# Optimization experiments

Measured on AMD Instinct MI355X. Metric: run time of the kernel, lower is better.

## Reference

```python
import jax, jax.numpy as jnp
import numpy as np

D_MODEL = 1024
D_K = 1024
B = 4
T = 2048

def setup_inputs() -> dict:
    key = jax.random.key(0)
    k_x, k_q, k_k, k_v = jax.random.split(key, 4)
    s = 1.0 / np.sqrt(D_MODEL)
    return {
        "x": jax.random.normal(k_x, (B, T, D_MODEL), dtype=jnp.float32),
        "Wq": jax.random.normal(k_q, (D_MODEL, D_K), dtype=jnp.float32) * s,
        "Wk": jax.random.normal(k_k, (D_MODEL, D_K), dtype=jnp.float32) * s,
        "Wv": jax.random.normal(k_v, (D_MODEL, D_K), dtype=jnp.float32) * s,
    }

def reference(x, Wq, Wk, Wv):
    # x: (B, T, d_model); Wq/Wk/Wv: (d_model, d_k)
    Q = jnp.einsum('btd,dk->btk', x, Wq)
    K = jnp.einsum('btd,dk->btk', x, Wk)
    V = jnp.einsum('btd,dk->btk', x, Wv)
    scale = 1.0 / jnp.sqrt(jnp.asarray(D_K, dtype=x.dtype))
    scores = jnp.einsum('bqk,bsk->bqs', Q, K) * scale  # (B, T, T)
    t = scores.shape[1]
    causal = jnp.triu(jnp.ones((t, t), dtype=bool), k=1)  # True above diagonal
    scores = jnp.where(causal[None, :, :], jnp.asarray(-jnp.inf, dtype=scores.dtype), scores)
    weights = jax.nn.softmax(scores, axis=-1)
    # dropout p=0.0 -> identity
    return jnp.einsum('bqs,bsk->bqk', weights, V)
```

## Files before the change

kernel.cpp:

```cpp
#include <hip/hip_runtime.h>
#include <cstdint>

typedef __attribute__((ext_vector_type(4))) float f32x4;
typedef __attribute__((ext_vector_type(8))) __bf16 bf16x8;
typedef __attribute__((ext_vector_type(8))) unsigned short u16x8;

__device__ __forceinline__ unsigned short f2bf(float f) {
    union { float f; unsigned u; } v; v.f = f;
    unsigned u = v.u + 0x7FFFu + ((v.u >> 16) & 1u);
    return (unsigned short)(u >> 16);
}
__device__ __forceinline__ float bf2f(unsigned short h) {
    union { unsigned u; float f; } v; v.u = ((unsigned)h) << 16;
    return v.f;
}

__device__ __forceinline__ void gld_lds16(const void* g, void* l) {
    auto gp = reinterpret_cast<const __attribute__((address_space(1))) unsigned int*>(
        reinterpret_cast<uintptr_t>(g));
    auto lp = reinterpret_cast<__attribute__((address_space(3))) unsigned int*>(
        reinterpret_cast<uintptr_t>(l));
    __builtin_amdgcn_global_load_lds(gp, lp, 16, 0, 0);
}

template<int BF16OUT>
__device__ __forceinline__ void gemm_core(
    const unsigned short* A, int lda,
    const unsigned short* B, int ldb,
    void* C, int ldc,
    int ktiles, float scale,
    unsigned short* lA, unsigned short* lB)
{
    const int t = threadIdx.x;
    const int l = t & 63;
    const int w = t >> 6;
    const int wr = w >> 1, wc = w & 1;

    f32x4 acc[4][4];
#pragma unroll
    for (int i = 0; i < 4; ++i)
#pragma unroll
        for (int j = 0; j < 4; ++j)
#pragma unroll
            for (int e = 0; e < 4; ++e) acc[i][j][e] = 0.f;

    const int srow = t >> 3;
    const int schunk = t & 7;

    for (int kt = 0; kt < ktiles; ++kt) {
        const int k0 = kt << 6;
#pragma unroll
        for (int p = 0; p < 4; ++p) {
            const int row = (p << 5) + srow;
            const int sc = schunk ^ (row & 7);
            gld_lds16(A + (size_t)row * lda + k0 + (sc << 3), lA + (p << 11) + (t << 3));
            gld_lds16(B + (size_t)row * ldb + k0 + (sc << 3), lB + (p << 11) + (t << 3));
        }
        __syncthreads();
#pragma unroll
        for (int kk = 0; kk < 2; ++kk) {
            bf16x8 af[4], bfr[4];
            const int c = (kk << 5) + ((l >> 4) << 3);
#pragma unroll
            for (int mf = 0; mf < 4; ++mf) {
                const int r = (wr << 6) + (mf << 4) + (l & 15);
                const int ad = ((r << 6) + c) ^ ((r & 7) << 3);
                af[mf] = *(const bf16x8*)(lA + ad);
            }
#pragma unroll
            for (int nf = 0; nf < 4; ++nf) {
                const int r = (wc << 6) + (nf << 4) + (l & 15);
                const int ad = ((r << 6) + c) ^ ((r & 7) << 3);
                bfr[nf] = *(const bf16x8*)(lB + ad);
            }
#pragma unroll
            for (int mf = 0; mf < 4; ++mf)
#pragma unroll
                for (int nf = 0; nf < 4; ++nf)
                    acc[mf][nf] = __builtin_amdgcn_mfma_f32_16x16x32_bf16(
                        af[mf], bfr[nf], acc[mf][nf], 0, 0, 0);
        }
        __syncthreads();
    }

#pragma unroll
    for (int mf = 0; mf < 4; ++mf)
#pragma unroll
        for (int nf = 0; nf < 4; ++nf)
#pragma unroll
            for (int j = 0; j < 4; ++j) {
                const int row = (wr << 6) + (mf << 4) + ((l >> 4) << 2) + j;
                const int col = (wc << 6) + (nf << 4) + (l & 15);
                const float v = acc[mf][nf][j] * scale;
                if (BF16OUT)
                    ((unsigned short*)C)[(size_t)row * ldc + col] = f2bf(v);
                else
                    ((float*)C)[(size_t)row * ldc + col] = v;
            }
}

__global__ __launch_bounds__(256) void k_gemm_proj(
    const unsigned short* __restrict__ xb, const unsigned short* __restrict__ wt,
    unsigned short* __restrict__ out, float scale)
{
    __shared__ unsigned short lA[8192], lB[8192];
    gemm_core<1>(xb + (size_t)blockIdx.y * 128 * 1024, 1024,
                 wt + (size_t)blockIdx.x * 128 * 1024, 1024,
                 out + (size_t)blockIdx.y * 128 * 1024 + blockIdx.x * 128, 1024,
                 16, scale, lA, lB);
}

__global__ __launch_bounds__(256) void k_gemm_vt(
    const unsigned short* __restrict__ wtv, const unsigned short* __restrict__ xb,
    unsigned short* __restrict__ vt)
{
    __shared__ unsigned short lA[8192], lB[8192];
    gemm_core<1>(wtv + (size_t)blockIdx.y * 128 * 1024, 1024,
                 xb + (size_t)blockIdx.x * 128 * 1024, 1024,
                 vt + (size_t)blockIdx.y * 128 * 8192 + blockIdx.x * 128, 8192,
                 16, 1.0f, lA, lB);
}

__global__ __launch_bounds__(256) void k_scores(
    const unsigned short* __restrict__ Qb, const unsigned short* __restrict__ Kb,
    unsigned short* __restrict__ S)
{
    const int kt = blockIdx.x, qt = blockIdx.y, b = blockIdx.z;
    if (kt > qt) return;
    __shared__ unsigned short lA[8192], lB[8192];
    gemm_core<1>(Qb + ((size_t)b * 2048 + qt * 128) * 1024, 1024,
                 Kb + ((size_t)b * 2048 + kt * 128) * 1024, 1024,
                 S + (size_t)b * 4194304 + (size_t)qt * 128 * 2048 + kt * 128, 2048,
                 16, 1.0f, lA, lB);
}

__global__ __launch_bounds__(256) void k_pv(
    const unsigned short* __restrict__ P, const unsigned short* __restrict__ Vt,
    float* __restrict__ out)
{
    const int dn = blockIdx.x, qt = blockIdx.y, b = blockIdx.z;
    __shared__ unsigned short lA[8192], lB[8192];
    gemm_core<0>(P + (size_t)b * 4194304 + (size_t)qt * 128 * 2048, 2048,
                 Vt + (size_t)dn * 128 * 8192 + b * 2048, 8192,
                 out + ((size_t)b * 2048 + qt * 128) * 1024 + dn * 128, 1024,
                 (qt + 1) * 2, 1.0f, lA, lB);
}

__global__ __launch_bounds__(256) void k_cast_bf16(
    const float* __restrict__ in, unsigned short* __restrict__ out, int n8)
{
    const int i = blockIdx.x * 256 + threadIdx.x;
    if (i >= n8) return;
    const float4* p = (const float4*)in + (size_t)i * 2;
    const float4 a = p[0], b = p[1];
    u16x8 r;
    r[0] = f2bf(a.x); r[1] = f2bf(a.y); r[2] = f2bf(a.z); r[3] = f2bf(a.w);
    r[4] = f2bf(b.x); r[5] = f2bf(b.y); r[6] = f2bf(b.z); r[7] = f2bf(b.w);
    *(u16x8*)(out + (size_t)i * 8) = r;
}

__global__ __launch_bounds__(256) void k_transpose_cast(
    const float* __restrict__ in, unsigned short* __restrict__ out)
{
    __shared__ float tile[32][33];
    const int bx = blockIdx.x * 32, by = blockIdx.y * 32;
    const int tx = threadIdx.x, ty = threadIdx.y;
    for (int r = ty; r < 32; r += 8)
        tile[r][tx] = in[(size_t)(by + r) * 1024 + bx + tx];
    __syncthreads();
    for (int r = ty; r < 32; r += 8)
        out[(size_t)(bx + r) * 1024 + by + tx] = f2bf(tile[tx][r]);
}

__global__ __launch_bounds__(256) void k_softmax(unsigned short* __restrict__ S)
{
    const int w = threadIdx.x >> 6, l = threadIdx.x & 63;
    const int r = blockIdx.x * 4 + w;
    const int b = r >> 11, lr = r & 2047;
    unsigned short* row = S + ((size_t)b << 22) + ((size_t)lr << 11);
    const int edge = ((lr >> 7) + 1) << 7;

    float v[32];
#pragma unroll
    for (int i = 0; i < 4; ++i) {
        const int c0 = (l << 3) + (i << 9);
        if (c0 < edge) {
            const u16x8 u = *(const u16x8*)(row + c0);
#pragma unroll
            for (int j = 0; j < 8; ++j)
                v[(i << 3) + j] = (c0 + j <= lr) ? bf2f(u[j]) : -3.0e38f;
        } else {
#pragma unroll
            for (int j = 0; j < 8; ++j) v[(i << 3) + j] = -3.0e38f;
        }
    }
    float m = v[0];
#pragma unroll
    for (int k = 1; k < 32; ++k) m = fmaxf(m, v[k]);
#pragma unroll
    for (int s = 32; s; s >>= 1) m = fmaxf(m, __shfl_xor(m, s, 64));
    float sum = 0.f;
#pragma unroll
    for (int k = 0; k < 32; ++k) { const float e = __expf(v[k] - m); v[k] = e; sum += e; }
#pragma unroll
    for (int s = 32; s; s >>= 1) sum += __shfl_xor(sum, s, 64);
    const float inv = 1.f / sum;
#pragma unroll
    for (int i = 0; i < 4; ++i) {
        const int c0 = (l << 3) + (i << 9);
        if (c0 < edge) {
            u16x8 o;
#pragma unroll
            for (int j = 0; j < 8; ++j) o[j] = f2bf(v[(i << 3) + j] * inv);
            *(u16x8*)(row + c0) = o;
        }
    }
}

extern "C" void kernel_launch(void* const* d_in, const int* in_sizes, int n_in,
                              void* d_out, int out_size, void* d_ws, size_t ws_size,
                              hipStream_t stream)
{
    (void)in_sizes; (void)n_in; (void)out_size; (void)ws_size;
    const float* x  = (const float*)d_in[0];
    const float* Wq = (const float*)d_in[1];
    const float* Wk = (const float*)d_in[2];
    const float* Wv = (const float*)d_in[3];
    float* out = (float*)d_out;

    char* w = (char*)d_ws;
    unsigned short* xb  = (unsigned short*)(w);
    unsigned short* wtq = (unsigned short*)(w + 16777216);
    unsigned short* wtk = (unsigned short*)(w + 18874368);
    unsigned short* wtv = (unsigned short*)(w + 20971520);
    unsigned short* Qb  = (unsigned short*)(w + 23068672);
    unsigned short* Kb  = (unsigned short*)(w + 39845888);
    unsigned short* Vt  = (unsigned short*)(w + 56623104);
    unsigned short* S   = (unsigned short*)(w + 73400320);

    k_cast_bf16<<<4096, 256, 0, stream>>>(x, xb, 1048576);
    const dim3 tb(32, 8);
    k_transpose_cast<<<dim3(32, 32), tb, 0, stream>>>(Wq, wtq);
    k_transpose_cast<<<dim3(32, 32), tb, 0, stream>>>(Wk, wtk);
    k_transpose_cast<<<dim3(32, 32), tb, 0, stream>>>(Wv, wtv);

    k_gemm_proj<<<dim3(8, 64), 256, 0, stream>>>(xb, wtq, Qb, 0.03125f);
    k_gemm_proj<<<dim3(8, 64), 256, 0, stream>>>(xb, wtk, Kb, 1.0f);
    k_gemm_vt <<<dim3(64, 8), 256, 0, stream>>>(wtv, xb, Vt);

    k_scores  <<<dim3(16, 16, 4), 256, 0, stream>>>(Qb, Kb, S);
    k_softmax <<<2048, 256, 0, stream>>>(S);
    k_pv      <<<dim3(8, 16, 4), 256, 0, stream>>>(S, Vt, out);
}
```

Measured before the change: 267.9 us.

## Double-buffer GEMM core with 512 threads, fuse QK projection, balance PV tiles

```diff
diff --git a/kernel.cpp b/kernel.cpp
--- a/kernel.cpp
+++ b/kernel.cpp
@@ -24,11 +24,11 @@
 }
 
 template<int BF16OUT>
-__device__ __forceinline__ void gemm_core(
-    const unsigned short* A, int lda,
-    const unsigned short* B, int ldb,
-    void* C, int ldc,
-    int ktiles, float scale,
+__device__ __forceinline__ void gemm8(
+    const unsigned short* __restrict__ A, int lda,
+    const unsigned short* __restrict__ B, int ldb,
+    void* __restrict__ C, int ldc,
+    int ktiles,
     unsigned short* lA, unsigned short* lB)
 {
     const int t = threadIdx.x;
@@ -36,62 +36,74 @@
     const int w = t >> 6;
     const int wr = w >> 1, wc = w & 1;
 
-    f32x4 acc[4][4];
-#pragma unroll
-    for (int i = 0; i < 4; ++i)
+    f32x4 acc[2][4];
+#pragma unroll
+    for (int i = 0; i < 2; ++i)
 #pragma unroll
         for (int j = 0; j < 4; ++j)
 #pragma unroll
             for (int e = 0; e < 4; ++e) acc[i][j][e] = 0.f;
 
-    const int srow = t >> 3;
-    const int schunk = t & 7;
-
-    for (int kt = 0; kt < ktiles; ++kt) {
+    auto stage = [&](int p, int kt) {
         const int k0 = kt << 6;
 #pragma unroll
-        for (int p = 0; p < 4; ++p) {
-            const int row = (p << 5) + srow;
-            const int sc = schunk ^ (row & 7);
-            gld_lds16(A + (size_t)row * lda + k0 + (sc << 3), lA + (p << 11) + (t << 3));
-            gld_lds16(B + (size_t)row * ldb + k0 + (sc << 3), lB + (p << 11) + (t << 3));
-        }
-        __syncthreads();
+        for (int i = 0; i < 2; ++i) {
+            const int flat = t + (i << 9);
+            const int row = flat >> 3;
+            const int sc = (flat & 7) ^ (row & 7);
+            gld_lds16(A + (size_t)row * lda + k0 + (sc << 3), lA + (p << 13) + (flat << 3));
+            gld_lds16(B + (size_t)row * ldb + k0 + (sc << 3), lB + (p << 13) + (flat << 3));
+        }
+    };
+
+    auto compute = [&](int p) {
 #pragma unroll
         for (int kk = 0; kk < 2; ++kk) {
-            bf16x8 af[4], bfr[4];
+            bf16x8 af[2], bfr[4];
             const int c = (kk << 5) + ((l >> 4) << 3);
 #pragma unroll
-            for (int mf = 0; mf < 4; ++mf) {
-                const int r = (wr << 6) + (mf << 4) + (l & 15);
-                const int ad = ((r << 6) + c) ^ ((r & 7) << 3);
+            for (int mf = 0; mf < 2; ++mf) {
+                const int r = (wr << 5) + (mf << 4) + (l & 15);
+                const int ad = (((r << 6) + c) ^ ((r & 7) << 3)) + (p << 13);
                 af[mf] = *(const bf16x8*)(lA + ad);
             }
 #pragma unroll
             for (int nf = 0; nf < 4; ++nf) {
                 const int r = (wc << 6) + (nf << 4) + (l & 15);
-                const int ad = ((r << 6) + c) ^ ((r & 7) << 3);
+                const int ad = (((r << 6) + c) ^ ((r & 7) << 3)) + (p << 13);
                 bfr[nf] = *(const bf16x8*)(lB + ad);
             }
-#pragma unroll
-            for (int mf = 0; mf < 4; ++mf)
+            __builtin_amdgcn_s_setprio(1);
+#pragma unroll
+            for (int mf = 0; mf < 2; ++mf)
 #pragma unroll
                 for (int nf = 0; nf < 4; ++nf)
                     acc[mf][nf] = __builtin_amdgcn_mfma_f32_16x16x32_bf16(
                         af[mf], bfr[nf], acc[mf][nf], 0, 0, 0);
-        }
+            __builtin_amdgcn_s_setprio(0);
+        }
+    };
+
+    stage(0, 0);
+    __syncthreads();
+    int p = 0;
+    for (int kt = 0; kt < ktiles - 1; ++kt) {
+        stage(p ^ 1, kt + 1);
+        compute(p);
         __syncthreads();
+        p ^= 1;
     }
-
-#pragma unroll
-    for (int mf = 0; mf < 4; ++mf)
+    compute(p);
+
+#pragma unroll
+    for (int mf = 0; mf < 2; ++mf)
 #pragma unroll
         for (int nf = 0; nf < 4; ++nf)
 #pragma unroll
             for (int j = 0; j < 4; ++j) {
-                const int row = (wr << 6) + (mf << 4) + ((l >> 4) << 2) + j;
+                const int row = (wr << 5) + (mf << 4) + ((l >> 4) << 2) + j;
                 const int col = (wc << 6) + (nf << 4) + (l & 15);
-                const float v = acc[mf][nf][j] * scale;
+                const float v = acc[mf][nf][j];
                 if (BF16OUT)
                     ((unsigned short*)C)[(size_t)row * ldc + col] = f2bf(v);
                 else
@@ -99,51 +111,56 @@
             }
 }
 
-__global__ __launch_bounds__(256) void k_gemm_proj(
-    const unsigned short* __restrict__ xb, const unsigned short* __restrict__ wt,
-    unsigned short* __restrict__ out, float scale)
-{
-    __shared__ unsigned short lA[8192], lB[8192];
-    gemm_core<1>(xb + (size_t)blockIdx.y * 128 * 1024, 1024,
-                 wt + (size_t)blockIdx.x * 128 * 1024, 1024,
-                 out + (size_t)blockIdx.y * 128 * 1024 + blockIdx.x * 128, 1024,
-                 16, scale, lA, lB);
-}
-
-__global__ __launch_bounds__(256) void k_gemm_vt(
+__global__ __launch_bounds__(512, 4) void k_gemm_qk(
+    const unsigned short* __restrict__ xb, const unsigned short* __restrict__ wtqk,
+    unsigned short* __restrict__ qk)
+{
+    __shared__ unsigned short lA[16384], lB[16384];
+    gemm8<1>(xb + (size_t)blockIdx.y * 128 * 1024, 1024,
+             wtqk + (size_t)blockIdx.x * 128 * 1024, 1024,
+             qk + (size_t)blockIdx.y * 128 * 2048 + blockIdx.x * 128, 2048,
+             16, lA, lB);
+}
+
+__global__ __launch_bounds__(512, 4) void k_gemm_vt(
     const unsigned short* __restrict__ wtv, const unsigned short* __restrict__ xb,
     unsigned short* __restrict__ vt)
 {
-    __shared__ unsigned short lA[8192], lB[8192];
-    gemm_core<1>(wtv + (size_t)blockIdx.y * 128 * 1024, 1024,
-                 xb + (size_t)blockIdx.x * 128 * 1024, 1024,
-                 vt + (size_t)blockIdx.y * 128 * 8192 + blockIdx.x * 128, 8192,
-                 16, 1.0f, lA, lB);
-}
-
-__global__ __launch_bounds__(256) void k_scores(
-    const unsigned short* __restrict__ Qb, const unsigned short* __restrict__ Kb,
-    unsigned short* __restrict__ S)
+    __shared__ unsigned short lA[16384], lB[16384];
+    gemm8<1>(wtv + (size_t)blockIdx.y * 128 * 1024, 1024,
+             xb + (size_t)blockIdx.x * 128 * 1024, 1024,
+             vt + (size_t)blockIdx.y * 128 * 8192 + blockIdx.x * 128, 8192,
+             16, lA, lB);
+}
+
+__global__ __launch_bounds__(512, 4) void k_scores(
+    const unsigned short* __restrict__ qk, unsigned short* __restrict__ S)
 {
     const int kt = blockIdx.x, qt = blockIdx.y, b = blockIdx.z;
     if (kt > qt) return;
-    __shared__ unsigned short lA[8192], lB[8192];
-    gemm_core<1>(Qb + ((size_t)b * 2048 + qt * 128) * 1024, 1024,
-                 Kb + ((size_t)b * 2048 + kt * 128) * 1024, 1024,
-                 S + (size_t)b * 4194304 + (size_t)qt * 128 * 2048 + kt * 128, 2048,
-                 16, 1.0f, lA, lB);
-}
-
-__global__ __launch_bounds__(256) void k_pv(
+    __shared__ unsigned short lA[16384], lB[16384];
+    gemm8<1>(qk + ((size_t)b * 2048 + qt * 128) * 2048, 2048,
+             qk + ((size_t)b * 2048 + kt * 128) * 2048 + 1024, 2048,
+             S + (size_t)b * 4194304 + (size_t)qt * 128 * 2048 + kt * 128, 2048,
+             16, lA, lB);
+}
+
+__global__ __launch_bounds__(512, 4) void k_pv(
     const unsigned short* __restrict__ P, const unsigned short* __restrict__ Vt,
     float* __restrict__ out)
 {
-    const int dn = blockIdx.x, qt = blockIdx.y, b = blockIdx.z;
-    __shared__ unsigned short lA[8192], lB[8192];
-    gemm_core<0>(P + (size_t)b * 4194304 + (size_t)qt * 128 * 2048, 2048,
-                 Vt + (size_t)dn * 128 * 8192 + b * 2048, 8192,
-                 out + ((size_t)b * 2048 + qt * 128) * 1024 + dn * 128, 1024,
-                 (qt + 1) * 2, 1.0f, lA, lB);
+    const int dn = blockIdx.x, pr = blockIdx.y, b = blockIdx.z;
+    __shared__ unsigned short lA[16384], lB[16384];
+    const int q1 = pr, q2 = 15 - pr;
+    gemm8<0>(P + (size_t)b * 4194304 + (size_t)q1 * 128 * 2048, 2048,
+             Vt + (size_t)dn * 128 * 8192 + b * 2048, 8192,
+             out + ((size_t)b * 2048 + q1 * 128) * 1024 + dn * 128, 1024,
+             (q1 + 1) * 2, lA, lB);
+    __syncthreads();
+    gemm8<0>(P + (size_t)b * 4194304 + (size_t)q2 * 128 * 2048, 2048,
+             Vt + (size_t)dn * 128 * 8192 + b * 2048, 8192,
+             out + ((size_t)b * 2048 + q2 * 128) * 1024 + dn * 128, 1024,
+             (q2 + 1) * 2, lA, lB);
 }
 
 __global__ __launch_bounds__(256) void k_cast_bf16(
@@ -159,17 +176,22 @@
     *(u16x8*)(out + (size_t)i * 8) = r;
 }
 
-__global__ __launch_bounds__(256) void k_transpose_cast(
-    const float* __restrict__ in, unsigned short* __restrict__ out)
+__global__ __launch_bounds__(256) void k_transpose3(
+    const float* __restrict__ Wq, const float* __restrict__ Wk, const float* __restrict__ Wv,
+    unsigned short* __restrict__ wtqk, unsigned short* __restrict__ wtv)
 {
     __shared__ float tile[32][33];
+    const int z = blockIdx.z;
+    const float* in = (z == 0) ? Wq : (z == 1) ? Wk : Wv;
+    unsigned short* out = (z < 2) ? (wtqk + (size_t)z * 1048576) : wtv;
+    const float s = (z == 0) ? 0.03125f : 1.0f;
     const int bx = blockIdx.x * 32, by = blockIdx.y * 32;
     const int tx = threadIdx.x, ty = threadIdx.y;
     for (int r = ty; r < 32; r += 8)
         tile[r][tx] = in[(size_t)(by + r) * 1024 + bx + tx];
     __syncthreads();
     for (int r = ty; r < 32; r += 8)
-        out[(size_t)(bx + r) * 1024 + by + tx] = f2bf(tile[tx][r]);
+        out[(size_t)(bx + r) * 1024 + by + tx] = f2bf(tile[tx][r] * s);
 }
 
 __global__ __launch_bounds__(256) void k_softmax(unsigned short* __restrict__ S)
@@ -229,26 +251,20 @@
     float* out = (float*)d_out;
 
     char* w = (char*)d_ws;
-    unsigned short* xb  = (unsigned short*)(w);
-    unsigned short* wtq = (unsigned short*)(w + 16777216);
-    unsigned short* wtk = (unsigned short*)(w + 18874368);
-    unsigned short* wtv = (unsigned short*)(w + 20971520);
-    unsigned short* Qb  = (unsigned short*)(w + 23068672);
-    unsigned short* Kb  = (unsigned short*)(w + 39845888);
-    unsigned short* Vt  = (unsigned short*)(w + 56623104);
-    unsigned short* S   = (unsigned short*)(w + 73400320);
+    unsigned short* xb   = (unsigned short*)(w);
+    unsigned short* wtqk = (unsigned short*)(w + 16777216);
+    unsigned short* wtv  = (unsigned short*)(w + 20971520);
+    unsigned short* QK   = (unsigned short*)(w + 23068672);
+    unsigned short* Vt   = (unsigned short*)(w + 56623104);
+    unsigned short* S    = (unsigned short*)(w + 73400320);
 
     k_cast_bf16<<<4096, 256, 0, stream>>>(x, xb, 1048576);
-    const dim3 tb(32, 8);
-    k_transpose_cast<<<dim3(32, 32), tb, 0, stream>>>(Wq, wtq);
-    k_transpose_cast<<<dim3(32, 32), tb, 0, stream>>>(Wk, wtk);
-    k_transpose_cast<<<dim3(32, 32), tb, 0, stream>>>(Wv, wtv);
-
-    k_gemm_proj<<<dim3(8, 64), 256, 0, stream>>>(xb, wtq, Qb, 0.03125f);
-    k_gemm_proj<<<dim3(8, 64), 256, 0, stream>>>(xb, wtk, Kb, 1.0f);
-    k_gemm_vt <<<dim3(64, 8), 256, 0, stream>>>(wtv, xb, Vt);
-
-    k_scores  <<<dim3(16, 16, 4), 256, 0, stream>>>(Qb, Kb, S);
-    k_softmax <<<2048, 256, 0, stream>>>(S);
-    k_pv      <<<dim3(8, 16, 4), 256, 0, stream>>>(S, Vt, out);
-}
+    k_transpose3<<<dim3(32, 32, 3), dim3(32, 8), 0, stream>>>(Wq, Wk, Wv, wtqk, wtv);
+
+    k_gemm_qk<<<dim3(16, 64), 512, 0, stream>>>(xb, wtqk, QK);
+    k_gemm_vt<<<dim3(64, 8), 512, 0, stream>>>(wtv, xb, Vt);
+
+    k_scores <<<dim3(16, 16, 4), 512, 0, stream>>>(QK, S);
+    k_softmax<<<2048, 256, 0, stream>>>(S);
+    k_pv     <<<dim3(8, 8, 4), 512, 0, stream>>>(S, Vt, out);
+}
```

Result: faster. 228.8 us (-14.6%).
